# Kernel optimization log

Measured on AMD Instinct MI355X. Metric: run time of the kernel, lower is better.

## Reference

```python
import jax, jax.numpy as jnp
import numpy as np

B, S, HID, NH = 4, 2048, 1024, 16
DH = HID // NH  # 64
SCALE = 1.0 / float(np.sqrt(DH))


def _linear_params(key, scale=0.02):
    kw, kb = jax.random.split(key)
    W = jax.random.normal(kw, (HID, HID), dtype=jnp.float32) * scale
    b = jax.random.normal(kb, (HID,), dtype=jnp.float32) * scale
    return W, b


def setup_inputs() -> dict:
    key = jax.random.key(0)
    ks = jax.random.split(key, 9)
    x = jax.random.normal(ks[0], (B, S, HID), dtype=jnp.float32)
    reasoning_mask = jax.random.uniform(ks[1], (B, S, 1, 1), dtype=jnp.float32)
    Wq, bq = _linear_params(ks[2])
    Wk, bk = _linear_params(ks[3])
    Wv, bv = _linear_params(ks[4])
    Wqr, bqr = _linear_params(ks[5])
    Wkr, bkr = _linear_params(ks[6])
    Wo, bo = _linear_params(ks[7])
    return {"x": x, "reasoning_mask": reasoning_mask,
            "Wq": Wq, "bq": bq, "Wk": Wk, "bk": bk, "Wv": Wv, "bv": bv,
            "Wqr": Wqr, "bqr": bqr, "Wkr": Wkr, "bkr": bkr, "Wo": Wo, "bo": bo}


def reference(x, reasoning_mask, Wq, bq, Wk, bk, Wv, bv, Wqr, bqr, Wkr, bkr, Wo, bo):
    # Projections: x @ W + b, then view (B, S, NH, DH)
    def proj(W, b):
        return (jnp.einsum('bsh,hd->bsd', x, W) + b).reshape(B, S, NH, DH)

    q = proj(Wq, bq)
    k = proj(Wk, bk)
    v = proj(Wv, bv)
    q_r = proj(Wqr, bqr)
    k_r = proj(Wkr, bkr)

    # Reasoning-gated blend of standard and reasoning projections
    q = q * (1.0 - reasoning_mask) + q_r * reasoning_mask
    k = k * (1.0 - reasoning_mask) + k_r * reasoning_mask

    # Faithful to source: matmul over the LAST two dims of (B,S,NH,DH),
    # i.e. per-token attention ACROSS HEADS -> scores shape (B,S,NH,NH)
    scores = jnp.einsum('bshd,bsed->bshe', q, k) * SCALE
    attn = jax.nn.softmax(scores, axis=-1)  # dropout is identity at eval
    out = jnp.einsum('bshe,bsed->bshd', attn, v)  # (B,S,NH,DH)

    # Faithful transpose(1,2) + contiguous view to (B, S, HID)
    out = jnp.transpose(out, (0, 2, 1, 3)).reshape(B, -1, HID)
    return jnp.einsum('bsh,hd->bsd', out, Wo) + bo
```

## Files before the change

### kernel.cpp

```cpp
#include <hip/hip_runtime.h>
#include <hip/hip_bf16.h>


typedef __attribute__((ext_vector_type(8))) short short8;
typedef __attribute__((ext_vector_type(4))) short short4v;
typedef __attribute__((ext_vector_type(4))) float f32x4;

#define HID 1024
#define NTOK 8192
#define WT_ELEMS (1024 * 1024)

__device__ __forceinline__ short f2bs(float f) {
  __hip_bfloat16 h = __float2bfloat16(f);
  return *reinterpret_cast<short*>(&h);
}
__device__ __forceinline__ float bs2f(short s) {
  __hip_bfloat16 h;
  *reinterpret_cast<short*>(&h) = s;
  return __bfloat162float(h);
}
__device__ __forceinline__ void gload16(const void* g, void* l) {
  __builtin_amdgcn_global_load_lds(
      (const __attribute__((address_space(1))) void*)g,
      (__attribute__((address_space(3))) void*)l, 16, 0, 0);
}

#define BAR() asm volatile("s_barrier" ::: "memory")
#define VMWAIT(N) asm volatile("s_waitcnt vmcnt(" #N ")" ::: "memory")
#define SCB __builtin_amdgcn_sched_barrier(0)
#define PRIO1 __builtin_amdgcn_s_setprio(1)
#define PRIO0 __builtin_amdgcn_s_setprio(0)
#define MFMA16x16 __builtin_amdgcn_mfma_f32_16x16x32_bf16

__global__ __launch_bounds__(256) void prep_kernel(
    const float* __restrict__ W0, const float* __restrict__ W1,
    const float* __restrict__ W2, const float* __restrict__ W3,
    const float* __restrict__ W4, const float* __restrict__ W5,
    const float* __restrict__ X, short* __restrict__ WT, short* __restrict__ XB)
{
  __shared__ short sT[64][68];
  const int bid = blockIdx.x, tid = threadIdx.x;
  if (bid < 1536) {
    const int z = bid >> 8, rem = bid & 255;
    const float* W = z == 0 ? W0 : z == 1 ? W1 : z == 2 ? W2 : z == 3 ? W3
                   : z == 4 ? W4 : W5;
    short* OUT = WT + (size_t)z * WT_ELEMS;
    const int k0 = (rem & 15) * 64, n0 = (rem >> 4) * 64;
    #pragma unroll
    for (int i = 0; i < 4; i++) {
      const int li = tid + i * 256;
      const int kr = li >> 4, c4 = (li & 15) << 2;
      const f32x4 wv = *reinterpret_cast<const f32x4*>(&W[(size_t)(k0 + kr) * HID + n0 + c4]);
      short4v s4;
      #pragma unroll
      for (int j = 0; j < 4; j++) s4[j] = f2bs(wv[j]);
      *reinterpret_cast<short4v*>(&sT[kr][c4]) = s4;
    }
    __syncthreads();
    #pragma unroll
    for (int i = 0; i < 4; i++) {
      const int li = tid + i * 256;
      const int nr = li >> 4, k4 = (li & 15) << 2;
      short4v o;
      #pragma unroll
      for (int j = 0; j < 4; j++) o[j] = sT[k4 + j][nr];
      const int kcol = (k0 + k4) ^ ((nr & 7) << 3);
      *reinterpret_cast<short4v*>(&OUT[(size_t)(n0 + nr) * HID + kcol]) = o;
    }
  } else {
    const int gid = (bid - 1536) * 256 + tid;
    const int row = gid >> 7, kc = (gid & 127) << 3;
    const f32x4 a = *reinterpret_cast<const f32x4*>(&X[(size_t)row * HID + kc]);
    const f32x4 b = *reinterpret_cast<const f32x4*>(&X[(size_t)row * HID + kc + 4]);
    short8 s;
    #pragma unroll
    for (int j = 0; j < 4; j++) { s[j] = f2bs(a[j]); s[4 + j] = f2bs(b[j]); }
    const int phys = (kc & ~63) | ((kc & 63) ^ ((row & 7) << 3));
    *reinterpret_cast<short8*>(&XB[(size_t)row * HID + phys]) = s;
  }
}

__global__ __launch_bounds__(512, 2) void gated8_kernel(
    const short* __restrict__ XB, const short* __restrict__ WTbase,
    const float* __restrict__ bq, const float* __restrict__ bqr,
    const float* __restrict__ bk, const float* __restrict__ bkr,
    const float* __restrict__ MASK,
    __hip_bfloat16* __restrict__ qg, __hip_bfloat16* __restrict__ kg)
{
  __shared__ short lA[2][256][64];
  __shared__ short lB1[2][128][64];
  __shared__ short lB2[2][128][64];

  const int d = blockIdx.x;
  const int bx = d & 31, byz = d >> 5;
  const int by = byz & 7, z = byz >> 3;

  const short* W1T = WTbase + (size_t)(2 * z) * WT_ELEMS;
  const short* W2T = W1T + WT_ELEMS;
  const float* B1b = z ? bk : bq;
  const float* B2b = z ? bkr : bqr;
  __hip_bfloat16* OUT = z ? kg : qg;

  const int m0 = bx * 256, n0 = by * 128;
  const int tid = threadIdx.x, lane = tid & 63, w = tid >> 6;
  const int wr = (w >> 1) * 64, wc = (w & 1) * 64;
  const int lrow = lane & 15, lkhi = (lane >> 4) << 3;
  const int swz = (lrow & 7) << 3;
  const int srow = lane >> 3, scol = (lane & 7) << 3;

  f32x4 acc1[4][4] = {}, acc2[4][4] = {};
  short8 bf1k[4], bf2k[4], bf1b[4];
  short8 afA0, afA1, afA2, afA3;
  short8 afB0, afB1, afB2, afB3;

  auto stA2 = [&](int slot, int kt, int i0) {
    const int k0 = kt * 64;
    #pragma unroll
    for (int i = 0; i < 2; i++) {
      const int chunk = w * 4 + i0 + i;
      gload16(&XB[(size_t)(m0 + chunk * 8 + srow) * HID + k0 + scol],
              &lA[slot][chunk * 8][0]);
    }
  };
  auto stB1s = [&](int slot, int kt) {
    const int k0 = kt * 64;
    #pragma unroll
    for (int i = 0; i < 2; i++) {
      const int chunk = w * 2 + i;
      gload16(&W1T[(size_t)(n0 + chunk * 8 + srow) * HID + k0 + scol],
              &lB1[slot][chunk * 8][0]);
    }
  };
  auto stB2s = [&](int slot, int kt) {
    const int k0 = kt * 64;
    #pragma unroll
    for (int i = 0; i < 2; i++) {
      const int chunk = w * 2 + i;
      gload16(&W2T[(size_t)(n0 + chunk * 8 + srow) * HID + k0 + scol],
              &lB2[slot][chunk * 8][0]);
    }
  };
  auto rdA = [&](int s, int m, int kk) -> short8 {
    const int lk = (kk * 32 + lkhi) ^ swz;
    return *reinterpret_cast<const short8*>(&lA[s][wr + m * 16 + lrow][lk]);
  };

#define RDB1(DST, S, KK)                                                              \
  _Pragma("unroll")                                                                   \
  for (int n = 0; n < 4; n++) {                                                       \
    const int lk = ((KK) * 32 + lkhi) ^ swz;                                          \
    DST[n] = *reinterpret_cast<const short8*>(&lB1[S][wc + n * 16 + lrow][lk]);       \
  }
#define RDB2(DST, S, KK)                                                              \
  _Pragma("unroll")                                                                   \
  for (int n = 0; n < 4; n++) {                                                       \
    const int lk = ((KK) * 32 + lkhi) ^ swz;                                          \
    DST[n] = *reinterpret_cast<const short8*>(&lB2[S][wc + n * 16 + lrow][lk]);       \
  }
#define MMC1(A0, A1, A2, A3, BF)                                          \
  _Pragma("unroll")                                                       \
  for (int n = 0; n < 4; n++) {                                           \
    acc1[0][n] = MFMA16x16(A0, BF[n], acc1[0][n], 0, 0, 0);               \
    acc1[1][n] = MFMA16x16(A1, BF[n], acc1[1][n], 0, 0, 0);               \
    acc1[2][n] = MFMA16x16(A2, BF[n], acc1[2][n], 0, 0, 0);               \
    acc1[3][n] = MFMA16x16(A3, BF[n], acc1[3][n], 0, 0, 0);               \
  }
#define MMC2(A0, A1, A2, A3, BF)                                          \
  _Pragma("unroll")                                                       \
  for (int n = 0; n < 4; n++) {                                           \
    acc2[0][n] = MFMA16x16(A0, BF[n], acc2[0][n], 0, 0, 0);               \
    acc2[1][n] = MFMA16x16(A1, BF[n], acc2[1][n], 0, 0, 0);               \
    acc2[2][n] = MFMA16x16(A2, BF[n], acc2[2][n], 0, 0, 0);               \
    acc2[3][n] = MFMA16x16(A3, BF[n], acc2[3][n], 0, 0, 0);               \
  }
#define GTILE(S, SN, TS)                                                 \
  afA0 = rdA(S, 0, 0); afA1 = rdA(S, 1, 0);                              \
  afA2 = rdA(S, 2, 0); afA3 = rdA(S, 3, 0);                              \
  RDB1(bf1k, S, 0);                                                      \
  RDB2(bf2k, S, 0);                                                      \
  afB0 = rdA(S, 0, 1); afB1 = rdA(S, 1, 1);                              \
  afB2 = rdA(S, 2, 1); afB3 = rdA(S, 3, 1);                              \
  RDB1(bf1b, S, 1);                                                      \
  stA2(SN, TS, 0); stA2(SN, TS, 2); stB1s(SN, TS); stB2s(SN, TS);        \
  SCB;                                                                   \
  PRIO1; MMC1(afA0, afA1, afA2, afA3, bf1k) PRIO0;                       \
  PRIO1; MMC2(afA0, afA1, afA2, afA3, bf2k) PRIO0;                       \
  RDB2(bf2k, S, 1);                                                      \
  PRIO1; MMC1(afB0, afB1, afB2, afB3, bf1b) PRIO0;                       \
  PRIO1; MMC2(afB0, afB1, afB2, afB3, bf2k) PRIO0;                       \
  VMWAIT(0);                                                             \
  BAR();

  stA2(0, 0, 0); stA2(0, 0, 2); stB1s(0, 0); stB2s(0, 0);
  VMWAIT(0);
  BAR();

  #pragma unroll 1
  for (int i = 0; i < 16; i++) {
    const int S = i & 1, SN = S ^ 1;
    const int TS = (i < 15) ? i + 1 : 15;
    GTILE(S, SN, TS)
  }
  VMWAIT(0);
#undef GTILE
#undef MMC1
#undef MMC2
#undef RDB1
#undef RDB2

  #pragma unroll
  for (int m = 0; m < 4; m++) {
    const int rbase = m0 + wr + m * 16 + ((lane >> 4) << 2);
    #pragma unroll
    for (int n = 0; n < 4; n++) {
      const int col = n0 + wc + n * 16 + lrow;
      const float bias1 = B1b[col];
      const float bias2 = B2b[col];
      #pragma unroll
      for (int r = 0; r < 4; r++) {
        const int row = rbase + r;
        const float mk = MASK[row];
        const float val = (acc1[m][n][r] + bias1) * (1.f - mk) +
                          (acc2[m][n][r] + bias2) * mk;
        OUT[(size_t)row * HID + col] = __float2bfloat16(val);
      }
    }
  }
}

template<bool OUTF32>
__global__ __launch_bounds__(512, 2) void plain8_kernel(
    const short* __restrict__ A, const short* __restrict__ WT,
    const float* __restrict__ BIAS, void* __restrict__ OUTv)
{
  __shared__ short lA[3][256][64];
  __shared__ short lB[3][128][64];

  const int d = blockIdx.x;
  const int bx = d & 31, by = d >> 5;

  const int m0 = bx * 256, n0 = by * 128;
  const int tid = threadIdx.x, lane = tid & 63, w = tid >> 6;
  const int wr = (w >> 1) * 64, wc = (w & 1) * 64;
  const int lrow = lane & 15, lkhi = (lane >> 4) << 3;
  const int swz = (lrow & 7) << 3;
  const int srow = lane >> 3, scol = (lane & 7) << 3;

  f32x4 acc[4][4] = {};
  short8 paf[2][4], pbf[2][4];

  auto stTrip = [&](int slot, int kt, int t) {
    const int k0 = kt * 64;
    if (t == 0) {
      #pragma unroll
      for (int i = 0; i < 3; i++) {
        const int chunk = w * 4 + i;
        gload16(&A[(size_t)(m0 + chunk * 8 + srow) * HID + k0 + scol],
                &lA[slot][chunk * 8][0]);
      }
    } else {
      const int chunk = w * 4 + 3;
      gload16(&A[(size_t)(m0 + chunk * 8 + srow) * HID + k0 + scol],
              &lA[slot][chunk * 8][0]);
      #pragma unroll
      for (int i = 0; i < 2; i++) {
        const int bchunk = w * 2 + i;
        gload16(&WT[(size_t)(n0 + bchunk * 8 + srow) * HID + k0 + scol],
                &lB[slot][bchunk * 8][0]);
      }
    }
  };

#define RDP(S, KK)                                                                    \
  _Pragma("unroll")                                                                   \
  for (int m = 0; m < 4; m++) {                                                       \
    const int lk = ((KK) * 32 + lkhi) ^ swz;                                          \
    paf[KK][m] = *reinterpret_cast<const short8*>(&lA[S][wr + m * 16 + lrow][lk]);    \
    pbf[KK][m] = *reinterpret_cast<const short8*>(&lB[S][wc + m * 16 + lrow][lk]);    \
  }
#define PMM16(KK)                                                                     \
  _Pragma("unroll")                                                                   \
  for (int m = 0; m < 4; m++)                                                         \
    _Pragma("unroll")                                                                 \
    for (int n = 0; n < 4; n++)                                                       \
      acc[m][n] = MFMA16x16(paf[KK][m], pbf[KK][n], acc[m][n], 0, 0, 0);

  stTrip(0, 0, 0); stTrip(0, 0, 1);
  stTrip(1, 1, 0); stTrip(1, 1, 1);
  VMWAIT(6);
  BAR();

  int s = 0, s2 = 2;
  #pragma unroll 1
  for (int t = 0; t < 16; t++) {
    const int TS = (t < 14) ? t + 2 : 15;
    RDP(s, 0)
    RDP(s, 1)
    stTrip(s2, TS, 0); stTrip(s2, TS, 1);
    SCB;
    PRIO1; PMM16(0) PRIO0;
    PRIO1; PMM16(1) PRIO0;
    VMWAIT(6);
    BAR();
    s = (s == 2) ? 0 : s + 1;
    s2 = (s2 == 2) ? 0 : s2 + 1;
  }
  VMWAIT(0);
#undef PMM16
#undef RDP

  #pragma unroll
  for (int m = 0; m < 4; m++) {
    const int rbase = m0 + wr + m * 16 + ((lane >> 4) << 2);
    #pragma unroll
    for (int n = 0; n < 4; n++) {
      const int col = n0 + wc + n * 16 + lrow;
      const float bias = BIAS[col];
      #pragma unroll
      for (int r = 0; r < 4; r++) {
        const float val = acc[m][n][r] + bias;
        const size_t oidx = (size_t)(rbase + r) * HID + col;
        if (OUTF32) ((float*)OUTv)[oidx] = val;
        else ((__hip_bfloat16*)OUTv)[oidx] = __float2bfloat16(val);
      }
    }
  }
}

__global__ __launch_bounds__(256) void attn_kernel(
    const __hip_bfloat16* __restrict__ Q, const __hip_bfloat16* __restrict__ K,
    const __hip_bfloat16* __restrict__ V, __hip_bfloat16* __restrict__ O)
{
  __shared__ short sP[4][16][32];
  const int tid = threadIdx.x, w = tid >> 6, lane = tid & 63;
  const int t = blockIdx.x * 4 + w;
  const int b = t >> 11, s = t & 2047;
  const size_t tb = (size_t)t * HID;
  const short* q = (const short*)Q;
  const short* k = (const short*)K;
  const short* v = (const short*)V;
  const int lrow = lane & 15, lk = lane >> 4;

  *reinterpret_cast<short8*>(&sP[w][lrow][lk * 8]) = short8{0,0,0,0,0,0,0,0};

  f32x4 sc4 = {0.f, 0.f, 0.f, 0.f};
  #pragma unroll
  for (int kk = 0; kk < 2; kk++) {
    const size_t off = tb + (size_t)lrow * 64 + kk * 32 + lk * 8;
    const short8 qf = *reinterpret_cast<const short8*>(&q[off]);
    const short8 kf = *reinterpret_cast<const short8*>(&k[off]);
    sc4 = MFMA16x16(qf, kf, sc4, 0, 0, 0);
  }

  float p[4];
  #pragma unroll
  for (int r = 0; r < 4; r++) {
    const float x = sc4[r] * 0.125f;
    float mx = x;
    mx = fmaxf(mx, __shfl_xor(mx, 1));
    mx = fmaxf(mx, __shfl_xor(mx, 2));
    mx = fmaxf(mx, __shfl_xor(mx, 4));
    mx = fmaxf(mx, __shfl_xor(mx, 8));
    const float e = __expf(x - mx);
    float sm = e;
    sm += __shfl_xor(sm, 1);
    sm += __shfl_xor(sm, 2);
    sm += __shfl_xor(sm, 4);
    sm += __shfl_xor(sm, 8);
    p[r] = e / sm;
  }

  #pragma unroll
  for (int r = 0; r < 4; r++)
    sP[w][lk * 4 + r][lrow] = f2bs(p[r]);
  asm volatile("s_waitcnt lgkmcnt(0)" ::: "memory");
  SCB;

  const short8 af = *reinterpret_cast<const short8*>(&sP[w][lrow][lk * 8]);
  const int row7 = (s >> 4) & 7;
  const size_t obase = ((size_t)b * 2048 + (s >> 4)) * HID + ((size_t)(s & 15) << 6);
  #pragma unroll
  for (int db = 0; db < 4; db++) {
    short8 bf = {0, 0, 0, 0, 0, 0, 0, 0};
    if (lane < 32) {
      #pragma unroll
      for (int j = 0; j < 8; j++)
        bf[j] = v[tb + (size_t)(lk * 8 + j) * 64 + db * 16 + lrow];
    }
    f32x4 o = {0.f, 0.f, 0.f, 0.f};
    o = MFMA16x16(af, bf, o, 0, 0, 0);
    #pragma unroll
    for (int r = 0; r < 4; r++) {
      const int h = lk * 4 + r;
      const int dd = db * 16 + lrow;
      O[obase + (size_t)h * 128 * HID + (dd ^ (row7 << 3))] = __float2bfloat16(o[r]);
    }
  }
}

extern "C" void kernel_launch(void* const* d_in, const int* in_sizes, int n_in,
                              void* d_out, int out_size, void* d_ws, size_t ws_size,
                              hipStream_t stream) {
  (void)in_sizes; (void)n_in; (void)out_size; (void)ws_size;
  const float* x   = (const float*)d_in[0];
  const float* rm  = (const float*)d_in[1];
  const float* Wq  = (const float*)d_in[2];
  const float* bq  = (const float*)d_in[3];
  const float* Wk  = (const float*)d_in[4];
  const float* bk  = (const float*)d_in[5];
  const float* Wv  = (const float*)d_in[6];
  const float* bv  = (const float*)d_in[7];
  const float* Wqr = (const float*)d_in[8];
  const float* bqr = (const float*)d_in[9];
  const float* Wkr = (const float*)d_in[10];
  const float* bkr = (const float*)d_in[11];
  const float* Wo  = (const float*)d_in[12];
  const float* bo  = (const float*)d_in[13];

  char* ws = (char*)d_ws;
  short* wt = (short*)ws;
  __hip_bfloat16* qg = (__hip_bfloat16*)(ws + 12u * 1024 * 1024);
  __hip_bfloat16* vv = (__hip_bfloat16*)(ws + 28u * 1024 * 1024);
  __hip_bfloat16* ar = (__hip_bfloat16*)(ws + 44u * 1024 * 1024);
  short* xb = (short*)d_out;
  __hip_bfloat16* kg = (__hip_bfloat16*)((char*)d_out + 16u * 1024 * 1024);

  prep_kernel<<<dim3(5632), 256, 0, stream>>>(Wq, Wqr, Wk, Wkr, Wv, Wo, x, wt, xb);
  gated8_kernel<<<dim3(512), 512, 0, stream>>>(xb, wt, bq, bqr, bk, bkr, rm, qg, kg);
  plain8_kernel<false><<<dim3(256), 512, 0, stream>>>(xb, wt + (size_t)4 * WT_ELEMS, bv, vv);
  attn_kernel<<<dim3(NTOK / 4), 256, 0, stream>>>(qg, kg, vv, ar);
  plain8_kernel<true><<<dim3(256), 512, 0, stream>>>((const short*)ar,
                                                     wt + (size_t)5 * WT_ELEMS, bo, d_out);
}
```

Before: 137.8 us.

## Shrink gated GEMM tile to 128x128 with 256 threads, single-buffered LDS

Replaces the 256x128 double-buffered gated projection kernel (512 threads) with a 128x128 tile kernel of 256 threads and a single LDS buffer, doubling the grid to 1024 blocks. The global-to-LDS staging is no longer overlapped with MFMA compute inside a block. The kernel now relies on having more resident blocks per CU to hide latency. This trades intra-block software pipelining and A-tile reuse for smaller LDS footprint and higher occupancy, at the cost of more weight reloads and an exposed load wait each k-step.

Measured after the change: 190.7 us. 38.4% more time.

```diff
diff --git a/kernel.cpp b/kernel.cpp
--- a/kernel.cpp
+++ b/kernel.cpp
@@ -80,19 +80,19 @@
   }
 }
 
-__global__ __launch_bounds__(512, 2) void gated8_kernel(
+__global__ __launch_bounds__(256) void gatedm_kernel(
     const short* __restrict__ XB, const short* __restrict__ WTbase,
     const float* __restrict__ bq, const float* __restrict__ bqr,
     const float* __restrict__ bk, const float* __restrict__ bkr,
     const float* __restrict__ MASK,
     __hip_bfloat16* __restrict__ qg, __hip_bfloat16* __restrict__ kg)
 {
-  __shared__ short lA[2][256][64];
-  __shared__ short lB1[2][128][64];
-  __shared__ short lB2[2][128][64];
+  __shared__ short lA[128][64];
+  __shared__ short lB1[128][64];
+  __shared__ short lB2[128][64];
 
   const int d = blockIdx.x;
-  const int bx = d & 31, byz = d >> 5;
+  const int bx = d & 63, byz = d >> 6;
   const int by = byz & 7, z = byz >> 3;
 
   const short* W1T = WTbase + (size_t)(2 * z) * WT_ELEMS;
@@ -101,7 +101,7 @@
   const float* B2b = z ? bkr : bqr;
   __hip_bfloat16* OUT = z ? kg : qg;
 
-  const int m0 = bx * 256, n0 = by * 128;
+  const int m0 = bx * 128, n0 = by * 128;
   const int tid = threadIdx.x, lane = tid & 63, w = tid >> 6;
   const int wr = (w >> 1) * 64, wc = (w & 1) * 64;
   const int lrow = lane & 15, lkhi = (lane >> 4) << 3;
@@ -110,52 +110,45 @@
 
   f32x4 acc1[4][4] = {}, acc2[4][4] = {};
   short8 bf1k[4], bf2k[4], bf1b[4];
-  short8 afA0, afA1, afA2, afA3;
-  short8 afB0, afB1, afB2, afB3;
-
-  auto stA2 = [&](int slot, int kt, int i0) {
+  short8 afA0, afA1, afA2, afA3, afB0, afB1, afB2, afB3;
+
+  auto stage = [&](int kt) {
     const int k0 = kt * 64;
     #pragma unroll
-    for (int i = 0; i < 2; i++) {
-      const int chunk = w * 4 + i0 + i;
+    for (int i = 0; i < 4; i++) {
+      const int chunk = w * 4 + i;
       gload16(&XB[(size_t)(m0 + chunk * 8 + srow) * HID + k0 + scol],
-              &lA[slot][chunk * 8][0]);
+              &lA[chunk * 8][0]);
+    }
+    #pragma unroll
+    for (int i = 0; i < 4; i++) {
+      const int chunk = w * 4 + i;
+      gload16(&W1T[(size_t)(n0 + chunk * 8 + srow) * HID + k0 + scol],
+              &lB1[chunk * 8][0]);
+    }
+    #pragma unroll
+    for (int i = 0; i < 4; i++) {
+      const int chunk = w * 4 + i;
+      gload16(&W2T[(size_t)(n0 + chunk * 8 + srow) * HID + k0 + scol],
+              &lB2[chunk * 8][0]);
     }
   };
-  auto stB1s = [&](int slot, int kt) {
-    const int k0 = kt * 64;
-    #pragma unroll
-    for (int i = 0; i < 2; i++) {
-      const int chunk = w * 2 + i;
-      gload16(&W1T[(size_t)(n0 + chunk * 8 + srow) * HID + k0 + scol],
-              &lB1[slot][chunk * 8][0]);
-    }
+  auto rdA = [&](int m, int kk) -> short8 {
+    const int lk = (kk * 32 + lkhi) ^ swz;
+    return *reinterpret_cast<const short8*>(&lA[wr + m * 16 + lrow][lk]);
   };
-  auto stB2s = [&](int slot, int kt) {
-    const int k0 = kt * 64;
-    #pragma unroll
-    for (int i = 0; i < 2; i++) {
-      const int chunk = w * 2 + i;
-      gload16(&W2T[(size_t)(n0 + chunk * 8 + srow) * HID + k0 + scol],
-              &lB2[slot][chunk * 8][0]);
-    }
-  };
-  auto rdA = [&](int s, int m, int kk) -> short8 {
-    const int lk = (kk * 32 + lkhi) ^ swz;
-    return *reinterpret_cast<const short8*>(&lA[s][wr + m * 16 + lrow][lk]);
-  };
-
-#define RDB1(DST, S, KK)                                                              \
+
+#define RDB1(DST, KK)                                                                 \
   _Pragma("unroll")                                                                   \
   for (int n = 0; n < 4; n++) {                                                       \
     const int lk = ((KK) * 32 + lkhi) ^ swz;                                          \
-    DST[n] = *reinterpret_cast<const short8*>(&lB1[S][wc + n * 16 + lrow][lk]);       \
-  }
-#define RDB2(DST, S, KK)                                                              \
+    DST[n] = *reinterpret_cast<const short8*>(&lB1[wc + n * 16 + lrow][lk]);          \
+  }
+#define RDB2(DST, KK)                                                                 \
   _Pragma("unroll")                                                                   \
   for (int n = 0; n < 4; n++) {                                                       \
     const int lk = ((KK) * 32 + lkhi) ^ swz;                                          \
-    DST[n] = *reinterpret_cast<const short8*>(&lB2[S][wc + n * 16 + lrow][lk]);       \
+    DST[n] = *reinterpret_cast<const short8*>(&lB2[wc + n * 16 + lrow][lk]);          \
   }
 #define MMC1(A0, A1, A2, A3, BF)                                          \
   _Pragma("unroll")                                                       \
@@ -173,36 +166,25 @@
     acc2[2][n] = MFMA16x16(A2, BF[n], acc2[2][n], 0, 0, 0);               \
     acc2[3][n] = MFMA16x16(A3, BF[n], acc2[3][n], 0, 0, 0);               \
   }
-#define GTILE(S, SN, TS)                                                 \
-  afA0 = rdA(S, 0, 0); afA1 = rdA(S, 1, 0);                              \
-  afA2 = rdA(S, 2, 0); afA3 = rdA(S, 3, 0);                              \
-  RDB1(bf1k, S, 0);                                                      \
-  RDB2(bf2k, S, 0);                                                      \
-  afB0 = rdA(S, 0, 1); afB1 = rdA(S, 1, 1);                              \
-  afB2 = rdA(S, 2, 1); afB3 = rdA(S, 3, 1);                              \
-  RDB1(bf1b, S, 1);                                                      \
-  stA2(SN, TS, 0); stA2(SN, TS, 2); stB1s(SN, TS); stB2s(SN, TS);        \
-  SCB;                                                                   \
-  PRIO1; MMC1(afA0, afA1, afA2, afA3, bf1k) PRIO0;                       \
-  PRIO1; MMC2(afA0, afA1, afA2, afA3, bf2k) PRIO0;                       \
-  RDB2(bf2k, S, 1);                                                      \
-  PRIO1; MMC1(afB0, afB1, afB2, afB3, bf1b) PRIO0;                       \
-  PRIO1; MMC2(afB0, afB1, afB2, afB3, bf2k) PRIO0;                       \
-  VMWAIT(0);                                                             \
-  BAR();
-
-  stA2(0, 0, 0); stA2(0, 0, 2); stB1s(0, 0); stB2s(0, 0);
-  VMWAIT(0);
-  BAR();
 
   #pragma unroll 1
-  for (int i = 0; i < 16; i++) {
-    const int S = i & 1, SN = S ^ 1;
-    const int TS = (i < 15) ? i + 1 : 15;
-    GTILE(S, SN, TS)
-  }
-  VMWAIT(0);
-#undef GTILE
+  for (int kt = 0; kt < 16; kt++) {
+    stage(kt);
+    VMWAIT(0);
+    BAR();
+    afA0 = rdA(0, 0); afA1 = rdA(1, 0); afA2 = rdA(2, 0); afA3 = rdA(3, 0);
+    RDB1(bf1k, 0);
+    RDB2(bf2k, 0);
+    afB0 = rdA(0, 1); afB1 = rdA(1, 1); afB2 = rdA(2, 1); afB3 = rdA(3, 1);
+    RDB1(bf1b, 1);
+    SCB;
+    PRIO1; MMC1(afA0, afA1, afA2, afA3, bf1k) PRIO0;
+    PRIO1; MMC2(afA0, afA1, afA2, afA3, bf2k) PRIO0;
+    RDB2(bf2k, 1);
+    PRIO1; MMC1(afB0, afB1, afB2, afB3, bf1b) PRIO0;
+    PRIO1; MMC2(afB0, afB1, afB2, afB3, bf2k) PRIO0;
+    BAR();
+  }
 #undef MMC1
 #undef MMC2
 #undef RDB1
@@ -426,7 +408,7 @@
   __hip_bfloat16* kg = (__hip_bfloat16*)((char*)d_out + 16u * 1024 * 1024);
 
   prep_kernel<<<dim3(5632), 256, 0, stream>>>(Wq, Wqr, Wk, Wkr, Wv, Wo, x, wt, xb);
-  gated8_kernel<<<dim3(512), 512, 0, stream>>>(xb, wt, bq, bqr, bk, bkr, rm, qg, kg);
+  gatedm_kernel<<<dim3(1024), 256, 0, stream>>>(xb, wt, bq, bqr, bk, bkr, rm, qg, kg);
   plain8_kernel<false><<<dim3(256), 512, 0, stream>>>(xb, wt + (size_t)4 * WT_ELEMS, bv, vv);
   attn_kernel<<<dim3(NTOK / 4), 256, 0, stream>>>(qg, kg, vv, ar);
   plain8_kernel<true><<<dim3(256), 512, 0, stream>>>((const short*)ar,
```

## Triple-buffer activation tiles in gated projection GEMM to prefetch two steps ahead

Applied to the files above, without the earlier changes.

The activation (A) tile buffer in the gated Q/K projection kernel grows from two LDS slots to three and is loaded two K-steps ahead. The weight tiles stay double-buffered and one step ahead. The end-of-iteration wait drops from vmcnt(0) to vmcnt(4), so the newest A-tile loads can stay in flight across the barrier, which hides more global-load latency. The cost is 160KB of LDS per block, which limits the kernel to one block per CU, and a more delicate load-ordering scheme.

Result: no change. 135.5 us (median of 3 runs) (-1.6%).

```diff
diff --git a/kernel.cpp b/kernel.cpp
--- a/kernel.cpp
+++ b/kernel.cpp
@@ -80,14 +80,14 @@
   }
 }
 
-__global__ __launch_bounds__(512, 2) void gated8_kernel(
+__global__ __launch_bounds__(512, 2) void gated3_kernel(
     const short* __restrict__ XB, const short* __restrict__ WTbase,
     const float* __restrict__ bq, const float* __restrict__ bqr,
     const float* __restrict__ bk, const float* __restrict__ bkr,
     const float* __restrict__ MASK,
     __hip_bfloat16* __restrict__ qg, __hip_bfloat16* __restrict__ kg)
 {
-  __shared__ short lA[2][256][64];
+  __shared__ short lA[3][256][64];
   __shared__ short lB1[2][128][64];
   __shared__ short lB2[2][128][64];
 
@@ -110,14 +110,13 @@
 
   f32x4 acc1[4][4] = {}, acc2[4][4] = {};
   short8 bf1k[4], bf2k[4], bf1b[4];
-  short8 afA0, afA1, afA2, afA3;
-  short8 afB0, afB1, afB2, afB3;
-
-  auto stA2 = [&](int slot, int kt, int i0) {
+  short8 afA0, afA1, afA2, afA3, afB0, afB1, afB2, afB3;
+
+  auto stA4 = [&](int slot, int kt) {
     const int k0 = kt * 64;
     #pragma unroll
-    for (int i = 0; i < 2; i++) {
-      const int chunk = w * 4 + i0 + i;
+    for (int i = 0; i < 4; i++) {
+      const int chunk = w * 4 + i;
       gload16(&XB[(size_t)(m0 + chunk * 8 + srow) * HID + k0 + scol],
               &lA[slot][chunk * 8][0]);
     }
@@ -173,36 +172,35 @@
     acc2[2][n] = MFMA16x16(A2, BF[n], acc2[2][n], 0, 0, 0);               \
     acc2[3][n] = MFMA16x16(A3, BF[n], acc2[3][n], 0, 0, 0);               \
   }
-#define GTILE(S, SN, TS)                                                 \
-  afA0 = rdA(S, 0, 0); afA1 = rdA(S, 1, 0);                              \
-  afA2 = rdA(S, 2, 0); afA3 = rdA(S, 3, 0);                              \
-  RDB1(bf1k, S, 0);                                                      \
-  RDB2(bf2k, S, 0);                                                      \
-  afB0 = rdA(S, 0, 1); afB1 = rdA(S, 1, 1);                              \
-  afB2 = rdA(S, 2, 1); afB3 = rdA(S, 3, 1);                              \
-  RDB1(bf1b, S, 1);                                                      \
-  stA2(SN, TS, 0); stA2(SN, TS, 2); stB1s(SN, TS); stB2s(SN, TS);        \
-  SCB;                                                                   \
-  PRIO1; MMC1(afA0, afA1, afA2, afA3, bf1k) PRIO0;                       \
-  PRIO1; MMC2(afA0, afA1, afA2, afA3, bf2k) PRIO0;                       \
-  RDB2(bf2k, S, 1);                                                      \
-  PRIO1; MMC1(afB0, afB1, afB2, afB3, bf1b) PRIO0;                       \
-  PRIO1; MMC2(afB0, afB1, afB2, afB3, bf2k) PRIO0;                       \
-  VMWAIT(0);                                                             \
+
+  stB1s(0, 0); stB2s(0, 0); stA4(0, 0); stA4(1, 1);
+  VMWAIT(4);
   BAR();
 
-  stA2(0, 0, 0); stA2(0, 0, 2); stB1s(0, 0); stB2s(0, 0);
+  #pragma unroll 1
+  for (int t = 0; t < 16; t++) {
+    const int sa = t % 3, sb = t & 1;
+    const int ktB = (t < 15) ? t + 1 : 15;
+    const int ktA = (t < 14) ? t + 2 : 15;
+    afA0 = rdA(sa, 0, 0); afA1 = rdA(sa, 1, 0);
+    afA2 = rdA(sa, 2, 0); afA3 = rdA(sa, 3, 0);
+    RDB1(bf1k, sb, 0);
+    RDB2(bf2k, sb, 0);
+    afB0 = rdA(sa, 0, 1); afB1 = rdA(sa, 1, 1);
+    afB2 = rdA(sa, 2, 1); afB3 = rdA(sa, 3, 1);
+    RDB1(bf1b, sb, 1);
+    stB1s((t + 1) & 1, ktB); stB2s((t + 1) & 1, ktB);
+    stA4((t + 2) % 3, ktA);
+    SCB;
+    PRIO1; MMC1(afA0, afA1, afA2, afA3, bf1k) PRIO0;
+    PRIO1; MMC2(afA0, afA1, afA2, afA3, bf2k) PRIO0;
+    RDB2(bf2k, sb, 1);
+    PRIO1; MMC1(afB0, afB1, afB2, afB3, bf1b) PRIO0;
+    PRIO1; MMC2(afB0, afB1, afB2, afB3, bf2k) PRIO0;
+    VMWAIT(4);
+    BAR();
+  }
   VMWAIT(0);
-  BAR();
-
-  #pragma unroll 1
-  for (int i = 0; i < 16; i++) {
-    const int S = i & 1, SN = S ^ 1;
-    const int TS = (i < 15) ? i + 1 : 15;
-    GTILE(S, SN, TS)
-  }
-  VMWAIT(0);
-#undef GTILE
 #undef MMC1
 #undef MMC2
 #undef RDB1
@@ -426,7 +424,7 @@
   __hip_bfloat16* kg = (__hip_bfloat16*)((char*)d_out + 16u * 1024 * 1024);
 
   prep_kernel<<<dim3(5632), 256, 0, stream>>>(Wq, Wqr, Wk, Wkr, Wv, Wo, x, wt, xb);
-  gated8_kernel<<<dim3(512), 512, 0, stream>>>(xb, wt, bq, bqr, bk, bkr, rm, qg, kg);
+  gated3_kernel<<<dim3(512), 512, 0, stream>>>(xb, wt, bq, bqr, bk, bkr, rm, qg, kg);
   plain8_kernel<false><<<dim3(256), 512, 0, stream>>>(xb, wt + (size_t)4 * WT_ELEMS, bv, vv);
   attn_kernel<<<dim3(NTOK / 4), 256, 0, stream>>>(qg, kg, vv, ar);
   plain8_kernel<true><<<dim3(256), 512, 0, stream>>>((const short*)ar,
```
